# Optimization experiments

Hardware: AMD Instinct MI355X
Metric: run time of the kernel (lower is better)

The kernel has to match this reference:

```python
import jax, jax.numpy as jnp
import numpy as np

HIDDEN_SIZE = 1152
OUTPUT_LENGTH = 256
POSITIONS_PAD_VALUE = -1
GRID = 64  # 64x64 patch grid -> seq_len 4096


def setup_inputs() -> dict:
    key = jax.random.key(0)
    k1, k2 = jax.random.split(key)
    B, S, H = 8, GRID * GRID, HIDDEN_SIZE
    hidden_states = jax.random.normal(k1, (B, S, H), dtype=jnp.float32)
    positions_xy = jax.random.randint(k2, (B, S, 2), 0, GRID, dtype=jnp.int32)
    return {"hidden_states": hidden_states, "positions_xy": positions_xy}


def _pool(hidden_states, positions_xy):
    B, S, H = hidden_states.shape
    L = OUTPUT_LENGTH
    k = int(np.sqrt(S // L))
    assert k * k * L == S
    root = float(np.sqrt(HIDDEN_SIZE))

    padding = jnp.all(positions_xy == POSITIONS_PAD_VALUE, axis=-1)      # [B,S]
    safe = jnp.maximum(positions_xy, 0)                                   # [B,S,2]
    max_x = jnp.max(safe[..., 0], axis=-1, keepdims=True) + 1            # [B,1]
    kern = safe // k                                                      # [B,S,2]
    flat = kern[..., 0] + (max_x // k) * kern[..., 1]                     # [B,S] bin id in [0,L)
    w = jnp.where(padding, 0.0, 1.0 / float(k * k))                       # [B,S]

    def pool_one(xb, idxb, wb):
        # scatter-mean: equivalent to one-hot(idx)^T @ x with 1/k^2 weights
        pooled = jax.ops.segment_sum(xb * wb[:, None], idxb, num_segments=L)  # [L,H]
        wsum = jax.ops.segment_sum(wb, idxb, num_segments=L)                  # [L]
        return pooled, wsum > 0

    pooled, mask = jax.vmap(pool_one)(hidden_states.astype(jnp.float32), flat, w)
    pooled = pooled.astype(hidden_states.dtype) * root
    return pooled, mask


def reference(hidden_states, positions_xy):
    pooled, mask = _pool(hidden_states, positions_xy)
    return (pooled, mask)
```

## Files before the change

### kernel.cpp

```cpp
#include <hip/hip_runtime.h>

#define HD 1152
#define SQ 4096
#define NB 256
#define BT 8
#define KK 4

__global__ void __launch_bounds__(1024) k_prep(const int* __restrict__ pos,
                                               unsigned short* __restrict__ flat) {
    int b = blockIdx.x;
    int tid = threadIdx.x;
    const int4* p = (const int4*)(pos + (size_t)b * SQ * 2);
    int4 a = p[2 * tid];
    int4 c = p[2 * tid + 1];

    int mx = max(max(a.x, a.z), max(c.x, c.z));
    if (mx < 0) mx = 0;
    for (int off = 32; off > 0; off >>= 1)
        mx = max(mx, __shfl_down(mx, off, 64));
    __shared__ int sm[16];
    if ((tid & 63) == 0) sm[tid >> 6] = mx;
    __syncthreads();
    if (tid == 0) {
        int v = sm[0];
        #pragma unroll
        for (int i = 1; i < 16; ++i) v = max(v, sm[i]);
        sm[0] = v;
    }
    __syncthreads();
    const int mxq = (sm[0] + 1) / KK;

    #define FLATID(X, Y) ((unsigned short)((((X) == -1) && ((Y) == -1)) ? 0xFFFFu \
        : (unsigned)((max((X), 0) / KK) + mxq * (max((Y), 0) / KK))))
    ushort4 o;
    o.x = FLATID(a.x, a.y);
    o.y = FLATID(a.z, a.w);
    o.z = FLATID(c.x, c.y);
    o.w = FLATID(c.z, c.w);
    ((ushort4*)flat)[(size_t)b * (SQ / 4) + tid] = o;
    #undef FLATID
}

__global__ void __launch_bounds__(256) k_pool(const float* __restrict__ hs,
                                              const unsigned short* __restrict__ flat,
                                              float* __restrict__ out,
                                              float* __restrict__ mask) {
    int bl = blockIdx.x;
    int b = bl >> 8;
    unsigned l = (unsigned)(bl & (NB - 1));
    int tid = threadIdx.x;
    int wv = tid >> 6, lane = tid & 63;

    __shared__ unsigned short list[SQ];
    __shared__ int wcnt[4];

    const int tokbase = wv * 1024 + lane * 16;
    const unsigned short* f = flat + b * SQ;
    const uint4* fp = (const uint4*)(f + tokbase);
    uint4 q0 = fp[0];
    uint4 q1 = fp[1];

    unsigned w[8] = {q0.x, q0.y, q0.z, q0.w, q1.x, q1.y, q1.z, q1.w};
    unsigned m16 = 0;
    #pragma unroll
    for (int j = 0; j < 8; ++j) {
        if ((w[j] & 0xFFFFu) == l) m16 |= 1u << (2 * j);
        if ((w[j] >> 16) == l)     m16 |= 1u << (2 * j + 1);
    }
    int cnt = __popc(m16);

    int pre = cnt;
    #pragma unroll
    for (int off = 1; off < 64; off <<= 1) {
        int n = __shfl_up(pre, off, 64);
        if (lane >= off) pre += n;
    }
    if (lane == 63) wcnt[wv] = pre;
    int excl = pre - cnt;
    __syncthreads();

    int woff = 0;
    #pragma unroll
    for (int v = 0; v < 4; ++v) if (v < wv) woff += wcnt[v];
    int total = wcnt[0] + wcnt[1] + wcnt[2] + wcnt[3];

    int r = woff + excl;
    unsigned m = m16;
    while (m) {
        int j = __ffs(m) - 1;
        m &= m - 1;
        list[r++] = (unsigned short)(tokbase + j);
    }
    __syncthreads();

    float4 a0 = make_float4(0.f, 0.f, 0.f, 0.f);
    float4 a1 = make_float4(0.f, 0.f, 0.f, 0.f);
    const float* hb = hs + (size_t)b * SQ * HD;
    int i = 0;
    for (; i + 1 < total; i += 2) {
        const float4* r0 = (const float4*)(hb + (size_t)list[i] * HD);
        const float4* r1 = (const float4*)(hb + (size_t)list[i + 1] * HD);
        float4 v0 = r0[tid];
        float4 v1 = r1[tid];
        a0.x += v0.x; a0.y += v0.y; a0.z += v0.z; a0.w += v0.w;
        a0.x += v1.x; a0.y += v1.y; a0.z += v1.z; a0.w += v1.w;
        if (tid < HD / 4 - 256) {
            float4 u0 = r0[256 + tid];
            float4 u1 = r1[256 + tid];
            a1.x += u0.x; a1.y += u0.y; a1.z += u0.z; a1.w += u0.w;
            a1.x += u1.x; a1.y += u1.y; a1.z += u1.z; a1.w += u1.w;
        }
    }
    if (i < total) {
        const float4* r0 = (const float4*)(hb + (size_t)list[i] * HD);
        float4 v0 = r0[tid];
        a0.x += v0.x; a0.y += v0.y; a0.z += v0.z; a0.w += v0.w;
        if (tid < HD / 4 - 256) {
            float4 u0 = r0[256 + tid];
            a1.x += u0.x; a1.y += u0.y; a1.z += u0.z; a1.w += u0.w;
        }
    }

    const float scale = 2.1213203435596424f;
    float4* o = (float4*)(out + (size_t)bl * HD);
    a0.x *= scale; a0.y *= scale; a0.z *= scale; a0.w *= scale;
    o[tid] = a0;
    if (tid < HD / 4 - 256) {
        a1.x *= scale; a1.y *= scale; a1.z *= scale; a1.w *= scale;
        o[256 + tid] = a1;
    }
    if (tid == 0) mask[bl] = (total > 0) ? 1.0f : 0.0f;
}

extern "C" void kernel_launch(void* const* d_in, const int* in_sizes, int n_in,
                              void* d_out, int out_size, void* d_ws, size_t ws_size,
                              hipStream_t stream) {
    const float* hs = (const float*)d_in[0];
    const int* pos = (const int*)d_in[1];
    float* out = (float*)d_out;
    float* mask = out + (size_t)BT * NB * HD;

    unsigned short* flat = (unsigned short*)d_ws;

    k_prep<<<BT, 1024, 0, stream>>>(pos, flat);
    k_pool<<<BT * NB, 256, 0, stream>>>(hs, flat, out, mask);
}
```

Baseline: 35.90 us.

## Fuse bin-id preprocessing into pool kernel and unroll gather by four

Removes the separate prep kernel. Each pool block now reads the raw positions for its batch (32KB), computes the max-x reduction and the bin ids itself, and builds its token list. This saves one kernel launch and the workspace round trip, at the cost of every one of the 256 blocks per batch redundantly re-reading positions, mostly from L2. The accumulation loop is also unrolled to four rows per iteration so more loads are in flight.

```diff
diff --git a/kernel.cpp b/kernel.cpp
--- a/kernel.cpp
+++ b/kernel.cpp
@@ -6,43 +6,8 @@
 #define BT 8
 #define KK 4
 
-__global__ void __launch_bounds__(1024) k_prep(const int* __restrict__ pos,
-                                               unsigned short* __restrict__ flat) {
-    int b = blockIdx.x;
-    int tid = threadIdx.x;
-    const int4* p = (const int4*)(pos + (size_t)b * SQ * 2);
-    int4 a = p[2 * tid];
-    int4 c = p[2 * tid + 1];
-
-    int mx = max(max(a.x, a.z), max(c.x, c.z));
-    if (mx < 0) mx = 0;
-    for (int off = 32; off > 0; off >>= 1)
-        mx = max(mx, __shfl_down(mx, off, 64));
-    __shared__ int sm[16];
-    if ((tid & 63) == 0) sm[tid >> 6] = mx;
-    __syncthreads();
-    if (tid == 0) {
-        int v = sm[0];
-        #pragma unroll
-        for (int i = 1; i < 16; ++i) v = max(v, sm[i]);
-        sm[0] = v;
-    }
-    __syncthreads();
-    const int mxq = (sm[0] + 1) / KK;
-
-    #define FLATID(X, Y) ((unsigned short)((((X) == -1) && ((Y) == -1)) ? 0xFFFFu \
-        : (unsigned)((max((X), 0) / KK) + mxq * (max((Y), 0) / KK))))
-    ushort4 o;
-    o.x = FLATID(a.x, a.y);
-    o.y = FLATID(a.z, a.w);
-    o.z = FLATID(c.x, c.y);
-    o.w = FLATID(c.z, c.w);
-    ((ushort4*)flat)[(size_t)b * (SQ / 4) + tid] = o;
-    #undef FLATID
-}
-
-__global__ void __launch_bounds__(256) k_pool(const float* __restrict__ hs,
-                                              const unsigned short* __restrict__ flat,
+__global__ void __launch_bounds__(256) k_pool(const int* __restrict__ pos,
+                                              const float* __restrict__ hs,
                                               float* __restrict__ out,
                                               float* __restrict__ mask) {
     int bl = blockIdx.x;
@@ -53,19 +18,34 @@
 
     __shared__ unsigned short list[SQ];
     __shared__ int wcnt[4];
+    __shared__ int smax[4];
 
-    const int tokbase = wv * 1024 + lane * 16;
-    const unsigned short* f = flat + b * SQ;
-    const uint4* fp = (const uint4*)(f + tokbase);
-    uint4 q0 = fp[0];
-    uint4 q1 = fp[1];
+    const int tokbase = tid * 16;
+    const int4* pp = (const int4*)(pos + (size_t)b * SQ * 2) + tid * 8;
+    int4 q[8];
+    #pragma unroll
+    for (int j = 0; j < 8; ++j) q[j] = pp[j];
 
-    unsigned w[8] = {q0.x, q0.y, q0.z, q0.w, q1.x, q1.y, q1.z, q1.w};
+    int mx = 0;
+    #pragma unroll
+    for (int j = 0; j < 8; ++j) mx = max(mx, max(q[j].x, q[j].z));
+    #pragma unroll
+    for (int off = 32; off > 0; off >>= 1)
+        mx = max(mx, __shfl_down(mx, off, 64));
+    if (lane == 0) smax[wv] = mx;
+    __syncthreads();
+    const int mxq = (max(max(smax[0], smax[1]), max(smax[2], smax[3])) + 1) / KK;
+
     unsigned m16 = 0;
     #pragma unroll
     for (int j = 0; j < 8; ++j) {
-        if ((w[j] & 0xFFFFu) == l) m16 |= 1u << (2 * j);
-        if ((w[j] >> 16) == l)     m16 |= 1u << (2 * j + 1);
+        int x0 = q[j].x, y0 = q[j].y, x1 = q[j].z, y1 = q[j].w;
+        unsigned f0 = (unsigned)((max(x0, 0) >> 2) + mxq * (max(y0, 0) >> 2));
+        unsigned f1 = (unsigned)((max(x1, 0) >> 2) + mxq * (max(y1, 0) >> 2));
+        bool p0 = (x0 == -1) && (y0 == -1);
+        bool p1 = (x1 == -1) && (y1 == -1);
+        if (!p0 && f0 == l) m16 |= 1u << (2 * j);
+        if (!p1 && f1 == l) m16 |= 1u << (2 * j + 1);
     }
     int cnt = __popc(m16);
 
@@ -97,21 +77,26 @@
     float4 a1 = make_float4(0.f, 0.f, 0.f, 0.f);
     const float* hb = hs + (size_t)b * SQ * HD;
     int i = 0;
-    for (; i + 1 < total; i += 2) {
-        const float4* r0 = (const float4*)(hb + (size_t)list[i] * HD);
+    for (; i + 3 < total; i += 4) {
+        const float4* r0 = (const float4*)(hb + (size_t)list[i]     * HD);
         const float4* r1 = (const float4*)(hb + (size_t)list[i + 1] * HD);
-        float4 v0 = r0[tid];
-        float4 v1 = r1[tid];
-        a0.x += v0.x; a0.y += v0.y; a0.z += v0.z; a0.w += v0.w;
-        a0.x += v1.x; a0.y += v1.y; a0.z += v1.z; a0.w += v1.w;
+        const float4* r2 = (const float4*)(hb + (size_t)list[i + 2] * HD);
+        const float4* r3 = (const float4*)(hb + (size_t)list[i + 3] * HD);
+        float4 v0 = r0[tid], v1 = r1[tid], v2 = r2[tid], v3 = r3[tid];
+        a0.x += v0.x + v1.x + v2.x + v3.x;
+        a0.y += v0.y + v1.y + v2.y + v3.y;
+        a0.z += v0.z + v1.z + v2.z + v3.z;
+        a0.w += v0.w + v1.w + v2.w + v3.w;
         if (tid < HD / 4 - 256) {
-            float4 u0 = r0[256 + tid];
-            float4 u1 = r1[256 + tid];
-            a1.x += u0.x; a1.y += u0.y; a1.z += u0.z; a1.w += u0.w;
-            a1.x += u1.x; a1.y += u1.y; a1.z += u1.z; a1.w += u1.w;
+            float4 u0 = r0[256 + tid], u1 = r1[256 + tid];
+            float4 u2 = r2[256 + tid], u3 = r3[256 + tid];
+            a1.x += u0.x + u1.x + u2.x + u3.x;
+            a1.y += u0.y + u1.y + u2.y + u3.y;
+            a1.z += u0.z + u1.z + u2.z + u3.z;
+            a1.w += u0.w + u1.w + u2.w + u3.w;
         }
     }
-    if (i < total) {
+    for (; i < total; ++i) {
         const float4* r0 = (const float4*)(hb + (size_t)list[i] * HD);
         float4 v0 = r0[tid];
         a0.x += v0.x; a0.y += v0.y; a0.z += v0.z; a0.w += v0.w;
@@ -140,8 +125,5 @@
     float* out = (float*)d_out;
     float* mask = out + (size_t)BT * NB * HD;
 
-    unsigned short* flat = (unsigned short*)d_ws;
-
-    k_prep<<<BT, 1024, 0, stream>>>(pos, flat);
-    k_pool<<<BT * NB, 256, 0, stream>>>(hs, flat, out, mask);
+    k_pool<<<BT * NB, 256, 0, stream>>>(pos, hs, out, mask);
 }
```

Measured after the change: 32.41 us (median of 2 runs). 1.11x faster.
